# Optimization experiments

Measured on AMD Instinct MI355X. Metric: run time of the kernel, lower is better.

The kernel has to match this reference:

```python
import jax, jax.numpy as jnp
import numpy as np

EPS = 1e-8  # F.cosine_similarity default eps


def setup_inputs() -> dict:
    key = jax.random.key(0)
    k1, = jax.random.split(key, 1)
    x = jax.random.normal(k1, (16384, 512), dtype=jnp.float32)
    w = jnp.float32(10.0)   # init_w parameter
    b = jnp.float32(-5.0)   # init_b parameter
    return {"x": x, "w": w, "b": b}


def reference(x, w, b):
    # x: [2N, D] interleaved (anchor, positive) embeddings
    anchor = x[0::2]    # [N, D]
    positive = x[1::2]  # [N, D]
    N = anchor.shape[0]

    # cosine similarity matrix: cos[i, j] = <pos_i, anc_j> / max(|pos_i||anc_j|, eps)
    # (normalize + GEMM instead of the O(N*D*N) broadcast)
    dots = jnp.einsum('id,jd->ij', positive, anchor)          # [N, N]
    pn = jnp.linalg.norm(positive, axis=1)                    # [N]
    an = jnp.linalg.norm(anchor, axis=1)                      # [N]
    denom = jnp.maximum(pn[:, None] * an[None, :], EPS)
    cos_sim = dots / denom

    logits = cos_sim * w + b                                  # [N, N]
    labels = jnp.arange(N)

    # CrossEntropyLoss (mean reduction)
    logp = jax.nn.log_softmax(logits, axis=1)
    nloss = -jnp.mean(logp[jnp.arange(N), labels])
    return nloss
```

## Files before the change

### kernel.cpp

```cpp
#include <hip/hip_runtime.h>
#include <hip/hip_bf16.h>

typedef __attribute__((ext_vector_type(8))) short short8;
typedef __attribute__((ext_vector_type(4))) float f32x4;

#define D 512
#define NT 8

typedef const __attribute__((address_space(1))) void gvoid;
typedef __attribute__((address_space(3))) void lvoid;

__device__ inline unsigned pack2f(float lo, float hi) {
    __hip_bfloat162 v = __float22bfloat162_rn(make_float2(lo, hi));
    union { __hip_bfloat162 h; unsigned u; } cv;
    cv.h = v;
    return cv.u;
}

__device__ inline int4 pack8f(const float4& v0, const float4& v1, float sc) {
    int4 r;
    r.x = (int)pack2f(v0.x * sc, v0.y * sc);
    r.y = (int)pack2f(v0.z * sc, v0.w * sc);
    r.z = (int)pack2f(v1.x * sc, v1.y * sc);
    r.w = (int)pack2f(v1.z * sc, v1.w * sc);
    return r;
}

__global__ __launch_bounds__(512) void norm_kernel(
    const float* __restrict__ x,
    float* __restrict__ diag, float* __restrict__ sumexp,
    __hip_bfloat16* __restrict__ Pn, __hip_bfloat16* __restrict__ An)
{
    const int t = threadIdx.x;
    const int i = blockIdx.x * 8 + (t >> 6);
    const int lane = t & 63;
    const float4* ap = (const float4*)(x + (size_t)(2 * i) * D);
    const float4* pp = (const float4*)(x + (size_t)(2 * i + 1) * D);
    float4 a0 = ap[lane * 2], a1 = ap[lane * 2 + 1];
    float4 p0 = pp[lane * 2], p1 = pp[lane * 2 + 1];
    float ssa = a0.x*a0.x + a0.y*a0.y + a0.z*a0.z + a0.w*a0.w
              + a1.x*a1.x + a1.y*a1.y + a1.z*a1.z + a1.w*a1.w;
    float ssp = p0.x*p0.x + p0.y*p0.y + p0.z*p0.z + p0.w*p0.w
              + p1.x*p1.x + p1.y*p1.y + p1.z*p1.z + p1.w*p1.w;
    float dt  = p0.x*a0.x + p0.y*a0.y + p0.z*a0.z + p0.w*a0.w
              + p1.x*a1.x + p1.y*a1.y + p1.z*a1.z + p1.w*a1.w;
#pragma unroll
    for (int m = 1; m < 64; m <<= 1) {
        ssa += __shfl_xor(ssa, m);
        ssp += __shfl_xor(ssp, m);
        dt  += __shfl_xor(dt, m);
    }
    float an = sqrtf(ssa), pn = sqrtf(ssp);
    float ia = 1.0f / fmaxf(an, 1e-30f);
    float ip = 1.0f / fmaxf(pn, 1e-30f);
    if (lane == 0) {
        diag[i] = dt / fmaxf(pn * an, 1e-8f);
        sumexp[i] = 0.0f;
    }
    int4 wp_, wa_;
    wp_ = pack8f(make_float4(p0.x,p0.y,p0.z,p0.w), make_float4(p1.x,p1.y,p1.z,p1.w), ip);
    wa_ = pack8f(make_float4(a0.x,a0.y,a0.z,a0.w), make_float4(a1.x,a1.y,a1.z,a1.w), ia);
    ((int4*)(Pn + (size_t)i * D))[lane] = wp_;
    ((int4*)(An + (size_t)i * D))[lane] = wa_;
}

__global__ __launch_bounds__(512, 2) void gemm_lse_256(
    const __hip_bfloat16* __restrict__ Pn, const __hip_bfloat16* __restrict__ An,
    const float* __restrict__ wp, float* __restrict__ sumexp, int nbx)
{
    __shared__ __align__(16) unsigned char lds[131072];

    const int t = threadIdx.x;
    const int lane = t & 63, w = t >> 6;
    const int wm = w >> 2, wn = w & 3;
    const int l15 = lane & 15, lhi = lane >> 4;
    const int swz = (l15 & 7) << 4;
    const int kb0 = lhi * 16, kb1 = 64 + lhi * 16;

    const int nwg = nbx * nbx;
    const int cpx = nwg >> 3;
    const int bid = blockIdx.x;
    const int wgid = (bid & 7) * cpx + (bid >> 3);
    const int brow = (wgid / nbx) * 256;
    const int bcol = (wgid % nbx) * 256;

    const float wv = *wp;
    const float s = fabsf(wv);

    const int o_0 = t * 16, o_1 = t * 16 + 8192;
    const int rl0 = o_0 >> 7, rl1 = o_1 >> 7;
    const int ss0 = ((o_0 >> 4) & 7) ^ (rl0 & 7);
    const int ss1 = ((o_1 >> 4) & 7) ^ (rl1 & 7);

    const __hip_bfloat16* pa[2][2];
    const __hip_bfloat16* pb[2][2];
#pragma unroll
    for (int hf = 0; hf < 2; ++hf) {
        pa[hf][0] = Pn + (size_t)(brow + hf * 128 + rl0) * D + ss0 * 8;
        pa[hf][1] = Pn + (size_t)(brow + hf * 128 + rl1) * D + ss1 * 8;
        pb[hf][0] = An + (size_t)(bcol + hf * 128 + rl0) * D + ss0 * 8;
        pb[hf][1] = An + (size_t)(bcol + hf * 128 + rl1) * D + ss1 * 8;
    }

    auto stage = [&](int dn) {
        unsigned char* lA = lds + dn * 32768;
        unsigned char* lB = lds + 65536 + dn * 32768;
#pragma unroll
        for (int hf = 0; hf < 2; ++hf) {
            __builtin_amdgcn_global_load_lds((gvoid*)pa[hf][0], (lvoid*)(lA + hf * 16384 + o_0), 16, 0, 0);
            __builtin_amdgcn_global_load_lds((gvoid*)pa[hf][1], (lvoid*)(lA + hf * 16384 + o_1), 16, 0, 0);
            __builtin_amdgcn_global_load_lds((gvoid*)pb[hf][0], (lvoid*)(lB + hf * 16384 + o_0), 16, 0, 0);
            __builtin_amdgcn_global_load_lds((gvoid*)pb[hf][1], (lvoid*)(lB + hf * 16384 + o_1), 16, 0, 0);
            pa[hf][0] += 64; pa[hf][1] += 64;
            pb[hf][0] += 64; pb[hf][1] += 64;
        }
    };

    f32x4 acc[8][4];
#pragma unroll
    for (int mi = 0; mi < 8; ++mi)
#pragma unroll
        for (int ni = 0; ni < 4; ++ni)
#pragma unroll
            for (int j = 0; j < 4; ++j) acc[mi][ni][j] = 0.0f;

    stage(0);
    asm volatile("s_waitcnt vmcnt(0)" ::: "memory");
    __builtin_amdgcn_s_barrier();

    short8 a[2][4], b0[2][2], b1[2][2];

    for (int tn = 0; tn < NT; ++tn) {
        const int c = tn & 1;
        const unsigned char* lAc = lds + c * 32768 + wm * 16384 + l15 * 128;
        const unsigned char* lBc = lds + 65536 + c * 32768 + (wn >> 1) * 16384 + ((wn & 1) * 64 + l15) * 128;

#pragma unroll
        for (int mi = 0; mi < 4; ++mi) {
            a[0][mi] = *(const short8*)(lAc + mi * 2048 + (kb0 ^ swz));
            a[1][mi] = *(const short8*)(lAc + mi * 2048 + (kb1 ^ swz));
        }
#pragma unroll
        for (int nf = 0; nf < 2; ++nf) {
            b0[0][nf] = *(const short8*)(lBc + nf * 2048 + (kb0 ^ swz));
            b0[1][nf] = *(const short8*)(lBc + nf * 2048 + (kb1 ^ swz));
        }
        if (tn < NT - 1) stage(c ^ 1);
        __builtin_amdgcn_s_barrier();
        __builtin_amdgcn_s_setprio(1);
#pragma unroll
        for (int ks = 0; ks < 2; ++ks)
#pragma unroll
            for (int mi = 0; mi < 4; ++mi)
#pragma unroll
                for (int nf = 0; nf < 2; ++nf)
                    acc[mi][nf] = __builtin_amdgcn_mfma_f32_16x16x32_bf16(a[ks][mi], b0[ks][nf], acc[mi][nf], 0, 0, 0);
        __builtin_amdgcn_s_setprio(0);
        __builtin_amdgcn_s_barrier();

#pragma unroll
        for (int nf = 0; nf < 2; ++nf) {
            b1[0][nf] = *(const short8*)(lBc + 4096 + nf * 2048 + (kb0 ^ swz));
            b1[1][nf] = *(const short8*)(lBc + 4096 + nf * 2048 + (kb1 ^ swz));
        }
        __builtin_amdgcn_s_barrier();
        __builtin_amdgcn_s_setprio(1);
#pragma unroll
        for (int ks = 0; ks < 2; ++ks)
#pragma unroll
            for (int mi = 0; mi < 4; ++mi)
#pragma unroll
                for (int nf = 0; nf < 2; ++nf)
                    acc[mi][2 + nf] = __builtin_amdgcn_mfma_f32_16x16x32_bf16(a[ks][mi], b1[ks][nf], acc[mi][2 + nf], 0, 0, 0);
        __builtin_amdgcn_s_setprio(0);
        __builtin_amdgcn_s_barrier();

#pragma unroll
        for (int mi = 0; mi < 4; ++mi) {
            a[0][mi] = *(const short8*)(lAc + 8192 + mi * 2048 + (kb0 ^ swz));
            a[1][mi] = *(const short8*)(lAc + 8192 + mi * 2048 + (kb1 ^ swz));
        }
        __builtin_amdgcn_s_barrier();
        __builtin_amdgcn_s_setprio(1);
#pragma unroll
        for (int ks = 0; ks < 2; ++ks)
#pragma unroll
            for (int mi = 0; mi < 4; ++mi)
#pragma unroll
                for (int nf = 0; nf < 2; ++nf)
                    acc[4 + mi][2 + nf] = __builtin_amdgcn_mfma_f32_16x16x32_bf16(a[ks][mi], b1[ks][nf], acc[4 + mi][2 + nf], 0, 0, 0);
        __builtin_amdgcn_s_setprio(0);
        __builtin_amdgcn_s_barrier();

        __builtin_amdgcn_s_setprio(1);
#pragma unroll
        for (int ks = 0; ks < 2; ++ks)
#pragma unroll
            for (int mi = 0; mi < 4; ++mi)
#pragma unroll
                for (int nf = 0; nf < 2; ++nf)
                    acc[4 + mi][nf] = __builtin_amdgcn_mfma_f32_16x16x32_bf16(a[ks][mi], b0[ks][nf], acc[4 + mi][nf], 0, 0, 0);
        __builtin_amdgcn_s_setprio(0);
        asm volatile("s_waitcnt vmcnt(0) lgkmcnt(0)" ::: "memory");
        __builtin_amdgcn_s_barrier();
    }

#pragma unroll
    for (int mi = 0; mi < 8; ++mi) {
#pragma unroll
        for (int j = 0; j < 4; ++j) {
            float v = 0.0f;
#pragma unroll
            for (int ni = 0; ni < 4; ++ni)
                v += __expf(acc[mi][ni][j] * wv - s);
            v += __shfl_xor(v, 1);
            v += __shfl_xor(v, 2);
            v += __shfl_xor(v, 4);
            v += __shfl_xor(v, 8);
            if (l15 == 0) {
                int row = brow + wm * 128 + mi * 16 + lhi * 4 + j;
                atomicAdd(&sumexp[row], v);
            }
        }
    }
}

__global__ __launch_bounds__(256, 2) void gemm_lse_small(
    const float* __restrict__ x,
    const float* __restrict__ pinv, const float* __restrict__ ainv,
    const float* __restrict__ wp, float* __restrict__ sumexp, int N)
{
    __shared__ __align__(16) unsigned char lds[81920];
    unsigned char* As = lds;
    unsigned char* Bs = lds + 65536;

    const int t = threadIdx.x;
    const int rb = blockIdx.y, cs = blockIdx.x;
    const int lane = t & 63, w = t >> 6;
    const int wr = w >> 1, wc = w & 1;
    const int l15 = lane & 15, lhi = lane >> 4;

    const int colsPer = N >> 3;
    const int CT = colsPer / 64;
    const int Q = CT * (D / 64);

    {
        int r = t >> 2;
        int kq = (t & 3) << 7;
        int grow = rb * 64 + r;
        const float4* src = (const float4*)(x + (size_t)(2 * grow + 1) * D);
        float sc = pinv[grow];
#pragma unroll
        for (int i2 = 0; i2 < 16; ++i2) {
            int k0 = kq + i2 * 8;
            float4 v0 = src[k0 >> 2], v1 = src[(k0 >> 2) + 1];
            *(int4*)(As + r * 1024 + ((k0 * 2) ^ ((r & 7) << 4))) = pack8f(v0, v1, sc);
        }
    }

    const int cl = t >> 2;
    const int kq = (t & 3) << 4;

    auto loadB = [&](int q, int4& oa, int4& ob) {
        int ct = q >> 3, kc = q & 7;
        int c = cs * colsPer + ct * 64 + cl;
        int k = kc * 64 + kq;
        const float4* src = (const float4*)(x + (size_t)(2 * c) * D + k);
        float sc = ainv[c];
        float4 v0 = src[0], v1 = src[1], v2 = src[2], v3 = src[3];
        oa = pack8f(v0, v1, sc);
        ob = pack8f(v2, v3, sc);
    };
    auto writeB = [&](int buf, const int4& oa, const int4& ob) {
        unsigned char* bb = Bs + buf * 8192 + cl * 128;
        int kb0 = kq * 2;
        *(int4*)(bb + (kb0 ^ ((cl & 7) << 4))) = oa;
        *(int4*)(bb + ((kb0 + 16) ^ ((cl & 7) << 4))) = ob;
    };

    const float wv = *wp;
    const float s = fabsf(wv);

    int4 ba, bb2;
    loadB(0, ba, bb2);
    __syncthreads();
    writeB(0, ba, bb2);
    __syncthreads();

    f32x4 acc[2][2];
    float rs[2][4];
#pragma unroll
    for (int mi = 0; mi < 2; ++mi) {
#pragma unroll
        for (int j = 0; j < 4; ++j) rs[mi][j] = 0.0f;
#pragma unroll
        for (int ni = 0; ni < 2; ++ni)
#pragma unroll
            for (int j = 0; j < 4; ++j) acc[mi][ni][j] = 0.0f;
    }

    for (int q = 0; q < Q; ++q) {
        const int kc = q & 7;
        const bool more = (q + 1 < Q);
        if (more) loadB(q + 1, ba, bb2);
        const unsigned char* Bp = Bs + (q & 1) * 8192;
#pragma unroll
        for (int ks = 0; ks < 2; ++ks) {
            int ka = kc * 64 + ks * 32 + lhi * 8;
            int ra0 = wr * 32 + l15, ra1 = ra0 + 16;
            short8 a0 = *(const short8*)(As + ra0 * 1024 + ((ka * 2) ^ ((ra0 & 7) << 4)));
            short8 a1 = *(const short8*)(As + ra1 * 1024 + ((ka * 2) ^ ((ra1 & 7) << 4)));
            int kb = ks * 32 + lhi * 8;
            int c0 = wc * 32 + l15, c1 = c0 + 16;
            short8 b0 = *(const short8*)(Bp + c0 * 128 + ((kb * 2) ^ ((c0 & 7) << 4)));
            short8 b1 = *(const short8*)(Bp + c1 * 128 + ((kb * 2) ^ ((c1 & 7) << 4)));
            acc[0][0] = __builtin_amdgcn_mfma_f32_16x16x32_bf16(a0, b0, acc[0][0], 0, 0, 0);
            acc[0][1] = __builtin_amdgcn_mfma_f32_16x16x32_bf16(a0, b1, acc[0][1], 0, 0, 0);
            acc[1][0] = __builtin_amdgcn_mfma_f32_16x16x32_bf16(a1, b0, acc[1][0], 0, 0, 0);
            acc[1][1] = __builtin_amdgcn_mfma_f32_16x16x32_bf16(a1, b1, acc[1][1], 0, 0, 0);
        }
        if (kc == 7) {
#pragma unroll
            for (int mi = 0; mi < 2; ++mi)
#pragma unroll
                for (int ni = 0; ni < 2; ++ni)
#pragma unroll
                    for (int j = 0; j < 4; ++j) {
                        rs[mi][j] += __expf(acc[mi][ni][j] * wv - s);
                        acc[mi][ni][j] = 0.0f;
                    }
        }
        if (more) {
            __syncthreads();
            writeB((q + 1) & 1, ba, bb2);
            __syncthreads();
        }
    }

#pragma unroll
    for (int mi = 0; mi < 2; ++mi)
#pragma unroll
        for (int j = 0; j < 4; ++j) {
            float v = rs[mi][j];
            v += __shfl_xor(v, 1);
            v += __shfl_xor(v, 2);
            v += __shfl_xor(v, 4);
            v += __shfl_xor(v, 8);
            if (l15 == 0) {
                int row = rb * 64 + wr * 32 + mi * 16 + lhi * 4 + j;
                atomicAdd(&sumexp[row], v);
            }
        }
}

__global__ __launch_bounds__(512) void norm_small(
    const float* __restrict__ x,
    float* __restrict__ pinv, float* __restrict__ ainv,
    float* __restrict__ diag, float* __restrict__ sumexp)
{
    const int t = threadIdx.x;
    const int i = blockIdx.x * 8 + (t >> 6);
    const int lane = t & 63;
    const float4* ap = (const float4*)(x + (size_t)(2 * i) * D);
    const float4* pp = (const float4*)(x + (size_t)(2 * i + 1) * D);
    float4 a0 = ap[lane * 2], a1 = ap[lane * 2 + 1];
    float4 p0 = pp[lane * 2], p1 = pp[lane * 2 + 1];
    float ssa = a0.x*a0.x + a0.y*a0.y + a0.z*a0.z + a0.w*a0.w
              + a1.x*a1.x + a1.y*a1.y + a1.z*a1.z + a1.w*a1.w;
    float ssp = p0.x*p0.x + p0.y*p0.y + p0.z*p0.z + p0.w*p0.w
              + p1.x*p1.x + p1.y*p1.y + p1.z*p1.z + p1.w*p1.w;
    float dt  = p0.x*a0.x + p0.y*a0.y + p0.z*a0.z + p0.w*a0.w
              + p1.x*a1.x + p1.y*a1.y + p1.z*a1.z + p1.w*a1.w;
#pragma unroll
    for (int m = 1; m < 64; m <<= 1) {
        ssa += __shfl_xor(ssa, m);
        ssp += __shfl_xor(ssp, m);
        dt  += __shfl_xor(dt, m);
    }
    float an = sqrtf(ssa), pn = sqrtf(ssp);
    if (lane == 0) {
        ainv[i] = 1.0f / fmaxf(an, 1e-30f);
        pinv[i] = 1.0f / fmaxf(pn, 1e-30f);
        diag[i] = dt / fmaxf(pn * an, 1e-8f);
        sumexp[i] = 0.0f;
    }
}

__global__ __launch_bounds__(1024) void finalize_kernel(
    const float* __restrict__ sumexp, const float* __restrict__ diag,
    const float* __restrict__ wp, float* __restrict__ out, int N)
{
    const int t = threadIdx.x;
    const float w = *wp;
    const float s = fabsf(w);
    float acc = 0.0f;
    for (int i = t; i < N; i += 1024)
        acc += s + logf(sumexp[i]) - w * diag[i];
#pragma unroll
    for (int m = 1; m < 64; m <<= 1) acc += __shfl_xor(acc, m);
    __shared__ float red[16];
    if ((t & 63) == 0) red[t >> 6] = acc;
    __syncthreads();
    if (t == 0) {
        float v = 0.0f;
#pragma unroll
        for (int i = 0; i < 16; ++i) v += red[i];
        out[0] = v / (float)N;
    }
}

extern "C" void kernel_launch(void* const* d_in, const int* in_sizes, int n_in,
                              void* d_out, int out_size, void* d_ws, size_t ws_size,
                              hipStream_t stream) {
    const float* x  = (const float*)d_in[0];
    const float* wp = (const float*)d_in[1];

    const int N = in_sizes[0] / (2 * D);

    char* ws = (char*)d_ws;
    size_t nf = (size_t)N * 4;
    float* pinv   = (float*)(ws);
    float* ainv   = (float*)(ws + nf);
    float* diag   = (float*)(ws + 2 * nf);
    float* sumexp = (float*)(ws + 3 * nf);
    size_t base = (4 * nf + 255) & ~(size_t)255;
    __hip_bfloat16* Pn = (__hip_bfloat16*)(ws + base);
    __hip_bfloat16* An = (__hip_bfloat16*)(ws + base + (size_t)N * D * 2);
    const bool cached = ws_size >= base + (size_t)N * D * 4;

    if (cached) {
        norm_kernel<<<N / 8, 512, 0, stream>>>(x, diag, sumexp, Pn, An);
        const int nbx = N / 256;
        gemm_lse_256<<<nbx * nbx, 512, 0, stream>>>(Pn, An, wp, sumexp, nbx);
    } else {
        norm_small<<<N / 8, 512, 0, stream>>>(x, pinv, ainv, diag, sumexp);
        dim3 grid(8, N / 64);
        gemm_lse_small<<<grid, 256, 0, stream>>>(x, pinv, ainv, wp, sumexp, N);
    }

    finalize_kernel<<<1, 1024, 0, stream>>>(sumexp, diag, wp, (float*)d_out, N);
}
```

Measured before the change: 223.7 us.

## Interleave global-to-LDS staging with MFMA phases using partial vmcnt waits

Splits the per-iteration tile prefetch into four quarter stages, each issued alongside one MFMA sub-block, and waits with vmcnt(4) instead of fully draining. This lets loads for the next K slice overlap compute instead of stalling at the end of each iteration. The last iteration is peeled out so its drains can be tuned separately. The warp-to-row mapping changes so that each 128-row half of A and B is loaded independently, with matching changes to the LDS offsets and the output row index. The finer-grained waits add synchronisation subtlety and a risk of reading incomplete LDS data.

```diff
diff --git a/kernel.cpp b/kernel.cpp
--- a/kernel.cpp
+++ b/kernel.cpp
@@ -92,29 +92,58 @@
     const int ss0 = ((o_0 >> 4) & 7) ^ (rl0 & 7);
     const int ss1 = ((o_1 >> 4) & 7) ^ (rl1 & 7);
 
-    const __hip_bfloat16* pa[2][2];
-    const __hip_bfloat16* pb[2][2];
-#pragma unroll
-    for (int hf = 0; hf < 2; ++hf) {
-        pa[hf][0] = Pn + (size_t)(brow + hf * 128 + rl0) * D + ss0 * 8;
-        pa[hf][1] = Pn + (size_t)(brow + hf * 128 + rl1) * D + ss1 * 8;
-        pb[hf][0] = An + (size_t)(bcol + hf * 128 + rl0) * D + ss0 * 8;
-        pb[hf][1] = An + (size_t)(bcol + hf * 128 + rl1) * D + ss1 * 8;
-    }
-
-    auto stage = [&](int dn) {
-        unsigned char* lA = lds + dn * 32768;
-        unsigned char* lB = lds + 65536 + dn * 32768;
-#pragma unroll
-        for (int hf = 0; hf < 2; ++hf) {
-            __builtin_amdgcn_global_load_lds((gvoid*)pa[hf][0], (lvoid*)(lA + hf * 16384 + o_0), 16, 0, 0);
-            __builtin_amdgcn_global_load_lds((gvoid*)pa[hf][1], (lvoid*)(lA + hf * 16384 + o_1), 16, 0, 0);
-            __builtin_amdgcn_global_load_lds((gvoid*)pb[hf][0], (lvoid*)(lB + hf * 16384 + o_0), 16, 0, 0);
-            __builtin_amdgcn_global_load_lds((gvoid*)pb[hf][1], (lvoid*)(lB + hf * 16384 + o_1), 16, 0, 0);
-            pa[hf][0] += 64; pa[hf][1] += 64;
-            pb[hf][0] += 64; pb[hf][1] += 64;
-        }
-    };
+    const __hip_bfloat16* g0[4];
+    const __hip_bfloat16* g1[4];
+    g0[0] = Pn + (size_t)(brow +   0 + rl0) * D + ss0 * 8;
+    g1[0] = Pn + (size_t)(brow +   0 + rl1) * D + ss1 * 8;
+    g0[1] = An + (size_t)(bcol +   0 + rl0) * D + ss0 * 8;
+    g1[1] = An + (size_t)(bcol +   0 + rl1) * D + ss1 * 8;
+    g0[2] = An + (size_t)(bcol + 128 + rl0) * D + ss0 * 8;
+    g1[2] = An + (size_t)(bcol + 128 + rl1) * D + ss1 * 8;
+    g0[3] = Pn + (size_t)(brow + 128 + rl0) * D + ss0 * 8;
+    g1[3] = Pn + (size_t)(brow + 128 + rl1) * D + ss1 * 8;
+
+    const int sbase[4] = { 0, 65536, 65536 + 16384, 16384 };
+
+#define STAGE(H, DN, KOFF) do {                                                            \
+        unsigned char* _d = lds + sbase[H] + (DN) * 32768;                                 \
+        __builtin_amdgcn_global_load_lds((gvoid*)(g0[H] + (KOFF)), (lvoid*)(_d + o_0), 16, 0, 0); \
+        __builtin_amdgcn_global_load_lds((gvoid*)(g1[H] + (KOFF)), (lvoid*)(_d + o_1), 16, 0, 0); \
+    } while (0)
+
+#define RDA(OFF) do {                                                                      \
+        _Pragma("unroll")                                                                  \
+        for (int mi = 0; mi < 4; ++mi) {                                                   \
+            a[0][mi] = *(const short8*)(lAc + (OFF) + mi * 2048 + (kb0 ^ swz));            \
+            a[1][mi] = *(const short8*)(lAc + (OFF) + mi * 2048 + (kb1 ^ swz));            \
+        }                                                                                  \
+    } while (0)
+
+#define RDB(BB, OFF) do {                                                                  \
+        _Pragma("unroll")                                                                  \
+        for (int nf = 0; nf < 2; ++nf) {                                                   \
+            BB[0][nf] = *(const short8*)(lBc + (OFF) + nf * 2048 + (kb0 ^ swz));           \
+            BB[1][nf] = *(const short8*)(lBc + (OFF) + nf * 2048 + (kb1 ^ swz));           \
+        }                                                                                  \
+    } while (0)
+
+#define MF(MB, NB, BB) do {                                                                \
+        __builtin_amdgcn_s_setprio(1);                                                     \
+        _Pragma("unroll")                                                                  \
+        for (int ks = 0; ks < 2; ++ks) {                                                   \
+            _Pragma("unroll")                                                              \
+            for (int mi = 0; mi < 4; ++mi) {                                               \
+                _Pragma("unroll")                                                          \
+                for (int nf = 0; nf < 2; ++nf)                                             \
+                    acc[(MB) + mi][(NB) + nf] = __builtin_amdgcn_mfma_f32_16x16x32_bf16(   \
+                        a[ks][mi], BB[ks][nf], acc[(MB) + mi][(NB) + nf], 0, 0, 0);        \
+            }                                                                              \
+        }                                                                                  \
+        __builtin_amdgcn_s_setprio(0);                                                     \
+    } while (0)
+
+#define LGKM0 do { asm volatile("s_waitcnt lgkmcnt(0)" ::: "memory");                      \
+                   __builtin_amdgcn_sched_barrier(0); } while (0)
 
     f32x4 acc[8][4];
 #pragma unroll
@@ -124,86 +153,87 @@
 #pragma unroll
             for (int j = 0; j < 4; ++j) acc[mi][ni][j] = 0.0f;
 
-    stage(0);
-    asm volatile("s_waitcnt vmcnt(0)" ::: "memory");
+    STAGE(0, 0, 0);
+    STAGE(1, 0, 0);
+    STAGE(2, 0, 0);
+    STAGE(3, 0, 0);
+    asm volatile("s_waitcnt vmcnt(4)" ::: "memory");
     __builtin_amdgcn_s_barrier();
 
     short8 a[2][4], b0[2][2], b1[2][2];
-
-    for (int tn = 0; tn < NT; ++tn) {
-        const int c = tn & 1;
-        const unsigned char* lAc = lds + c * 32768 + wm * 16384 + l15 * 128;
-        const unsigned char* lBc = lds + 65536 + c * 32768 + (wn >> 1) * 16384 + ((wn & 1) * 64 + l15) * 128;
-
-#pragma unroll
-        for (int mi = 0; mi < 4; ++mi) {
-            a[0][mi] = *(const short8*)(lAc + mi * 2048 + (kb0 ^ swz));
-            a[1][mi] = *(const short8*)(lAc + mi * 2048 + (kb1 ^ swz));
-        }
-#pragma unroll
-        for (int nf = 0; nf < 2; ++nf) {
-            b0[0][nf] = *(const short8*)(lBc + nf * 2048 + (kb0 ^ swz));
-            b0[1][nf] = *(const short8*)(lBc + nf * 2048 + (kb1 ^ swz));
-        }
-        if (tn < NT - 1) stage(c ^ 1);
-        __builtin_amdgcn_s_barrier();
-        __builtin_amdgcn_s_setprio(1);
-#pragma unroll
-        for (int ks = 0; ks < 2; ++ks)
-#pragma unroll
-            for (int mi = 0; mi < 4; ++mi)
-#pragma unroll
-                for (int nf = 0; nf < 2; ++nf)
-                    acc[mi][nf] = __builtin_amdgcn_mfma_f32_16x16x32_bf16(a[ks][mi], b0[ks][nf], acc[mi][nf], 0, 0, 0);
-        __builtin_amdgcn_s_setprio(0);
-        __builtin_amdgcn_s_barrier();
-
-#pragma unroll
-        for (int nf = 0; nf < 2; ++nf) {
-            b1[0][nf] = *(const short8*)(lBc + 4096 + nf * 2048 + (kb0 ^ swz));
-            b1[1][nf] = *(const short8*)(lBc + 4096 + nf * 2048 + (kb1 ^ swz));
-        }
-        __builtin_amdgcn_s_barrier();
-        __builtin_amdgcn_s_setprio(1);
-#pragma unroll
-        for (int ks = 0; ks < 2; ++ks)
-#pragma unroll
-            for (int mi = 0; mi < 4; ++mi)
-#pragma unroll
-                for (int nf = 0; nf < 2; ++nf)
-                    acc[mi][2 + nf] = __builtin_amdgcn_mfma_f32_16x16x32_bf16(a[ks][mi], b1[ks][nf], acc[mi][2 + nf], 0, 0, 0);
-        __builtin_amdgcn_s_setprio(0);
-        __builtin_amdgcn_s_barrier();
-
-#pragma unroll
-        for (int mi = 0; mi < 4; ++mi) {
-            a[0][mi] = *(const short8*)(lAc + 8192 + mi * 2048 + (kb0 ^ swz));
-            a[1][mi] = *(const short8*)(lAc + 8192 + mi * 2048 + (kb1 ^ swz));
-        }
-        __builtin_amdgcn_s_barrier();
-        __builtin_amdgcn_s_setprio(1);
-#pragma unroll
-        for (int ks = 0; ks < 2; ++ks)
-#pragma unroll
-            for (int mi = 0; mi < 4; ++mi)
-#pragma unroll
-                for (int nf = 0; nf < 2; ++nf)
-                    acc[4 + mi][2 + nf] = __builtin_amdgcn_mfma_f32_16x16x32_bf16(a[ks][mi], b1[ks][nf], acc[4 + mi][2 + nf], 0, 0, 0);
-        __builtin_amdgcn_s_setprio(0);
-        __builtin_amdgcn_s_barrier();
-
-        __builtin_amdgcn_s_setprio(1);
-#pragma unroll
-        for (int ks = 0; ks < 2; ++ks)
-#pragma unroll
-            for (int mi = 0; mi < 4; ++mi)
-#pragma unroll
-                for (int nf = 0; nf < 2; ++nf)
-                    acc[4 + mi][nf] = __builtin_amdgcn_mfma_f32_16x16x32_bf16(a[ks][mi], b0[ks][nf], acc[4 + mi][nf], 0, 0, 0);
-        __builtin_amdgcn_s_setprio(0);
-        asm volatile("s_waitcnt vmcnt(0) lgkmcnt(0)" ::: "memory");
-        __builtin_amdgcn_s_barrier();
-    }
+    const unsigned char* lAc;
+    const unsigned char* lBc;
+
+    for (int tn = 0; tn < NT - 1; ++tn) {
+        const int c = tn & 1, dn = c ^ 1;
+        const int koff = (tn + 1) * 64;
+        lAc = lds + c * 32768 + wm * 8192 + l15 * 128;
+        lBc = lds + 65536 + c * 32768 + wn * 4096 + l15 * 128;
+
+        RDA(0);
+        RDB(b0, 0);
+        STAGE(0, dn, koff);
+        __builtin_amdgcn_s_barrier();
+        LGKM0;
+        MF(0, 0, b0);
+        asm volatile("s_waitcnt vmcnt(4)" ::: "memory");
+        __builtin_amdgcn_s_barrier();
+
+        RDB(b1, 16384);
+        STAGE(1, dn, koff);
+        __builtin_amdgcn_s_barrier();
+        LGKM0;
+        MF(0, 2, b1);
+        asm volatile("s_waitcnt vmcnt(4)" ::: "memory");
+        __builtin_amdgcn_s_barrier();
+
+        RDA(16384);
+        STAGE(2, dn, koff);
+        __builtin_amdgcn_s_barrier();
+        LGKM0;
+        MF(4, 2, b1);
+        __builtin_amdgcn_s_barrier();
+
+        STAGE(3, dn, koff);
+        __builtin_amdgcn_s_barrier();
+        MF(4, 0, b0);
+        asm volatile("s_waitcnt vmcnt(4)" ::: "memory");
+        __builtin_amdgcn_s_barrier();
+    }
+
+    {
+        lAc = lds + 32768 + wm * 8192 + l15 * 128;
+        lBc = lds + 65536 + 32768 + wn * 4096 + l15 * 128;
+
+        RDA(0);
+        RDB(b0, 0);
+        __builtin_amdgcn_s_barrier();
+        LGKM0;
+        MF(0, 0, b0);
+        asm volatile("s_waitcnt vmcnt(2)" ::: "memory");
+        __builtin_amdgcn_s_barrier();
+
+        RDB(b1, 16384);
+        __builtin_amdgcn_s_barrier();
+        LGKM0;
+        MF(0, 2, b1);
+        asm volatile("s_waitcnt vmcnt(0)" ::: "memory");
+        __builtin_amdgcn_s_barrier();
+
+        RDA(16384);
+        __builtin_amdgcn_s_barrier();
+        LGKM0;
+        MF(4, 2, b1);
+        __builtin_amdgcn_s_barrier();
+
+        MF(4, 0, b0);
+    }
+
+#undef STAGE
+#undef RDA
+#undef RDB
+#undef MF
+#undef LGKM0
 
 #pragma unroll
     for (int mi = 0; mi < 8; ++mi) {
@@ -218,7 +248,7 @@
             v += __shfl_xor(v, 4);
             v += __shfl_xor(v, 8);
             if (l15 == 0) {
-                int row = brow + wm * 128 + mi * 16 + lhi * 4 + j;
+                int row = brow + (mi >> 2) * 128 + wm * 64 + (mi & 3) * 16 + lhi * 4 + j;
                 atomicAdd(&sumexp[row], v);
             }
         }
```

New measurement: 241.8 us. +8.1%, slower.
